# Optimization experiments

Measured on AMD Instinct MI355X. Metric: run time of the kernel, lower is better.

The kernel has to match this reference:

```python
import jax, jax.numpy as jnp
import numpy as np

Z1, COND, HID, NSTEP, B = 128, 12, 1024, 32, 4096


def setup_inputs() -> dict:
    key = jax.random.key(0)
    ks = jax.random.split(key, 10)
    s = 0.05  # init scale for learned params
    return {
        "z": jax.random.normal(ks[0], (B, Z1), jnp.float32),
        "condition": jax.random.uniform(ks[1], (B, NSTEP, COND), jnp.float32),
        "iteration": 1000,
        # nn.GRUCell params (gate order: r, z, n)
        "W_ih": jax.random.normal(ks[2], (3 * HID, Z1 + COND), jnp.float32) * s,
        "W_hh": jax.random.normal(ks[3], (3 * HID, HID), jnp.float32) * s,
        "b_ih": jax.random.normal(ks[4], (3 * HID,), jnp.float32) * s,
        "b_hh": jax.random.normal(ks[5], (3 * HID,), jnp.float32) * s,
        # linear_init_0
        "W_init": jax.random.normal(ks[6], (HID, Z1), jnp.float32) * s,
        "b_init": jax.random.normal(ks[7], (HID,), jnp.float32) * s,
        # linear_out_0
        "W_out": jax.random.normal(ks[8], (COND, HID), jnp.float32) * s,
        "b_out": jax.random.normal(ks[9], (COND,), jnp.float32) * s,
    }


def reference(z, condition, iteration, W_ih, W_hh, b_ih, b_hh, W_init, b_init, W_out, b_out):
    # Deterministic teacher-forcing path (training, eps=1): feedback at step i
    # is zeros for i=0, else condition[:, i-1, :]. iteration only affects the
    # stochastic eps schedule, which is dropped for determinism.
    del iteration
    b = z.shape[0]
    hx = jnp.tanh(z @ W_init.T + b_init)  # [B, H]
    feed = jnp.concatenate(
        [jnp.zeros((b, 1, COND), z.dtype), condition[:, :-1, :]], axis=1)  # [B, T, C]
    inputs = jnp.concatenate(
        [feed, jnp.broadcast_to(z[:, None, :], (b, NSTEP, z.shape[1]))], axis=-1)
    # precompute all input-to-hidden projections, time-major: [T, B, 3H]
    gi = jnp.einsum('bti,gi->tbg', inputs, W_ih) + b_ih

    def step(h, gi_t):
        gh = h @ W_hh.T + b_hh
        i_r, i_z, i_n = jnp.split(gi_t, 3, axis=-1)
        h_r, h_z, h_n = jnp.split(gh, 3, axis=-1)
        r = jax.nn.sigmoid(i_r + h_r)
        u = jax.nn.sigmoid(i_z + h_z)
        n = jnp.tanh(i_n + r * h_n)
        h_new = (1.0 - u) * n + u * h
        x = jax.nn.sigmoid(h_new @ W_out.T + b_out)  # [B, C]
        return h_new, x

    _, xs = jax.lax.scan(step, hx, gi)  # xs: [T, B, C]
    return jnp.transpose(xs, (1, 0, 2))  # [B, T, C]
```

## Files before the change

### kernel.cpp

```cpp
#include <hip/hip_runtime.h>
#include <stdint.h>

#define BB    4096
#define Z1D   128
#define CD    12
#define HD    1024
#define TT    32
#define N3H   3072
#define KAUG  1184
#define NGP   3168
#define NPH0B 1088

typedef __bf16 bf16;
typedef __bf16 bf16x2 __attribute__((ext_vector_type(2)));
typedef __bf16 bf16x8 __attribute__((ext_vector_type(8)));
typedef float  f32x4  __attribute__((ext_vector_type(4)));
typedef float  f4     __attribute__((ext_vector_type(4)));

typedef const __attribute__((address_space(1))) void* as1cv;
typedef __attribute__((address_space(3))) void* as3v;

__device__ __forceinline__ float sigm(float x){ return 1.0f/(1.0f+__expf(-x)); }
__device__ __forceinline__ float tanhfast(float x){ return 1.0f - 2.0f/(1.0f+__expf(2.0f*x)); }

__device__ __forceinline__ int rowOfN(int np, int& g){
  int jb = np/96; int r = np - jb*96; g = r>>5; int jl = r&31;
  return g*1024 + jb*32 + jl;
}

__global__ __launch_bounds__(256)
void prep_k(const float* __restrict__ z, const float* __restrict__ Wih,
            const float* __restrict__ Whh, const float* __restrict__ bih,
            const float* __restrict__ bhh, const float* __restrict__ Winit,
            const float* __restrict__ Wout,
            bf16* __restrict__ Wg, bf16* __restrict__ Wzn, bf16* __restrict__ Wi0,
            bf16* __restrict__ zbf, float* __restrict__ biasz,
            float* __restrict__ bhhn, float* __restrict__ bihn,
            bf16* __restrict__ A0, bf16* __restrict__ A1)
{
  const int N1 = NGP*KAUG;
  const int N2 = NPH0B*Z1D;
  const int N3 = NPH0B*Z1D;
  const int N4 = BB*Z1D;
  const int N5 = N3H;
  const int N6 = HD;
  const int N6b= HD;
  const int N7 = 2*BB*KAUG;
  int idx = blockIdx.x*256 + threadIdx.x;
  if (idx < N1){
    int np = idx/KAUG, k = idx - np*KAUG;
    float v = 0.0f;
    if (np < N3H){
      int g; int row = rowOfN(np, g);
      if (k < 1024) v = Whh[(size_t)row*HD + k];
      else if (g < 2){
        if (k < 1036)      v = Wih[(size_t)row*140 + (k-1024)];
        else if (k < 1164) v = Wih[(size_t)row*140 + 12 + (k-1036)];
      }
    } else {
      int c = np - N3H;
      if (c < CD && k < 1024) v = Wout[(size_t)c*HD + k];
    }
    Wg[idx] = (bf16)v;
    return;
  }
  idx -= N1;
  if (idx < N2){
    int jn = idx/Z1D, kk = idx - jn*Z1D;
    Wzn[idx] = (jn < HD) ? (bf16)Wih[(size_t)(2048+jn)*140 + 12 + kk] : (bf16)0.0f;
    return;
  }
  idx -= N2;
  if (idx < N3){
    int jn = idx/Z1D, kk = idx - jn*Z1D;
    Wi0[idx] = (jn < HD) ? (bf16)Winit[(size_t)jn*Z1D + kk] : (bf16)0.0f;
    return;
  }
  idx -= N3;
  if (idx < N4){ zbf[idx] = (bf16)z[idx]; return; }
  idx -= N4;
  if (idx < N5){
    int g; int row = rowOfN(idx, g);
    biasz[idx] = (g < 2) ? (bih[row] + bhh[row]) : 0.0f;
    return;
  }
  idx -= N5;
  if (idx < N6){ bhhn[idx] = bhh[2048 + idx]; return; }
  idx -= N6;
  if (idx < N6b){ bihn[idx] = bih[2048 + idx]; return; }
  idx -= N6b;
  if (idx < N7){
    int j = (idx < BB*KAUG) ? idx : idx - BB*KAUG;
    int b = j / KAUG, k = j - b*KAUG;
    bf16 v = (bf16)0.0f;
    if (k >= 1036 && k < 1164) v = (bf16)z[(size_t)b*Z1D + (k-1036)];
    if (idx < BB*KAUG) A0[j] = v; else A1[j] = v;
  }
}

template<int EP>
__global__ __launch_bounds__(256, 5)
void gemm_k(const bf16* __restrict__ A, int lda,
            const bf16* __restrict__ Bw, int ldb, int ksteps,
            const bf16* __restrict__ zpn, bf16* __restrict__ zpnw,
            const float* __restrict__ biasz, const float* __restrict__ bias1,
            const float* __restrict__ bhhn,
            const float* __restrict__ Wih, const float* __restrict__ cond,
            const bf16* __restrict__ Acur, bf16* __restrict__ Anext,
            const float* __restrict__ bout, float* __restrict__ outg, int t)
{
  __shared__ bf16 lA[2][128*32];
  __shared__ bf16 lB[2][96*32];
  const int tid = threadIdx.x, wid = tid>>6, lane = tid&63;
  const int l15 = lane&15, l4 = lane>>4;

  int bx, by;
  if constexpr (EP == 2){
    int bid = blockIdx.x;
    int x = bid & 7, k = bid >> 3;
    bx = k >> 2;
    by = x*4 + (k & 3);
  } else {
    bx = blockIdx.x; by = blockIdx.y;
  }
  const int n0 = bx*96, m0 = by*128;

  f32x4 acc[2][6];
  #pragma unroll
  for (int i=0;i<2;++i)
    #pragma unroll
    for (int j=0;j<6;++j) acc[i][j] = (f32x4){0.f,0.f,0.f,0.f};

  auto STAGE = [&](int buf, int ks){
    const int k0 = ks*32;
    const bf16* gA = A + (size_t)m0*lda + k0;
    #pragma unroll
    for (int r=0; r<2; ++r){
      int q = r*256 + tid;
      int row = q>>2, slot = q&3;
      int sg = slot ^ ((row>>1)&3);
      const bf16* gp = gA + (size_t)row*lda + sg*8;
      bf16* lp = &lA[buf][(size_t)(r*256 + wid*64)*8];
      __builtin_amdgcn_global_load_lds((as1cv)gp, (as3v)lp, 16, 0, 0);
    }
    const bf16* gB = Bw + (size_t)n0*ldb + k0;
    {
      int q = tid;
      int row = q>>2, slot = q&3;
      int sg = slot ^ ((row>>1)&3);
      const bf16* gp = gB + (size_t)row*ldb + sg*8;
      bf16* lp = &lB[buf][(size_t)(wid*64)*8];
      __builtin_amdgcn_global_load_lds((as1cv)gp, (as3v)lp, 16, 0, 0);
    }
    if (tid < 128){
      int q = 256 + tid;
      int row = q>>2, slot = q&3;
      int sg = slot ^ ((row>>1)&3);
      const bf16* gp = gB + (size_t)row*ldb + sg*8;
      bf16* lp = &lB[buf][(size_t)(256 + wid*64)*8];
      __builtin_amdgcn_global_load_lds((as1cv)gp, (as3v)lp, 16, 0, 0);
    }
  };

  const int sl = (l4 ^ ((l15>>1)&3))*8;

  int cur = 0;
  STAGE(0, 0);
  for (int ks=0; ks<ksteps; ++ks){
    __syncthreads();
    if (ks+1 < ksteps) STAGE(cur^1, ks+1);
    bf16x8 af0 = *(const bf16x8*)&lA[cur][(wid*32 +  0 + l15)*32 + sl];
    bf16x8 af1 = *(const bf16x8*)&lA[cur][(wid*32 + 16 + l15)*32 + sl];
    #pragma unroll
    for (int cf=0; cf<6; ++cf){
      bf16x8 bfr = *(const bf16x8*)&lB[cur][(cf*16 + l15)*32 + sl];
      acc[0][cf] = __builtin_amdgcn_mfma_f32_16x16x32_bf16(af0, bfr, acc[0][cf], 0,0,0);
      acc[1][cf] = __builtin_amdgcn_mfma_f32_16x16x32_bf16(af1, bfr, acc[1][cf], 0,0,0);
    }
    cur ^= 1;
  }

  const int rbase = m0 + wid*32 + l4*4;

  if constexpr (EP == 0){
    #pragma unroll
    for (int rf=0; rf<2; ++rf)
      #pragma unroll
      for (int cf=0; cf<6; ++cf){
        int jn = n0 + cf*16 + l15;
        if (jn < HD){
          float bi = bias1[jn];
          #pragma unroll
          for (int reg=0; reg<4; ++reg){
            int b = rbase + rf*16 + reg;
            zpnw[(size_t)b*HD + jn] = (bf16)(acc[rf][cf][reg] + bi);
          }
        }
      }
  }
  else if constexpr (EP == 1){
    #pragma unroll
    for (int rf=0; rf<2; ++rf)
      #pragma unroll
      for (int cf=0; cf<6; ++cf){
        int jn = n0 + cf*16 + l15;
        if (jn < HD){
          float bi = bias1[jn];
          #pragma unroll
          for (int reg=0; reg<4; ++reg){
            int b = rbase + rf*16 + reg;
            Anext[(size_t)b*KAUG + jn] = (bf16)tanhfast(acc[rf][cf][reg] + bi);
          }
        }
      }
  }
  else if (bx == 32){
    if (t > 0){
      int c = l15;
      if (c < CD){
        float bo = bout[c];
        #pragma unroll
        for (int rf=0; rf<2; ++rf){
          #pragma unroll
          for (int reg=0; reg<4; ++reg){
            int b = rbase + rf*16 + reg;
            outg[((size_t)b*TT + (t-1))*CD + c] = sigm(acc[rf][0][reg] + bo);
          }
        }
      }
    }
  }
  else {
    const int jblk = bx;
    float wfn[2][12];
    #pragma unroll
    for (int jf=0; jf<2; ++jf){
      int jn = jblk*32 + jf*16 + l15;
      const f4* wr = (const f4*)(Wih + (size_t)(2048 + jn)*140);
      f4 w0 = wr[0], w1 = wr[1], w2 = wr[2];
      #pragma unroll
      for (int c=0;c<4;++c){ wfn[jf][c]=w0[c]; wfn[jf][4+c]=w1[c]; wfn[jf][8+c]=w2[c]; }
    }
    #pragma unroll
    for (int rf=0; rf<2; ++rf){
      #pragma unroll
      for (int reg=0; reg<4; ++reg){
        int b = rbase + rf*16 + reg;
        const bf16* fr = Acur + (size_t)b*KAUG + 1024;
        bf16x8 f8 = *(const bf16x8*)fr;
        float fd[12];
        #pragma unroll
        for (int c=0;c<8;++c) fd[c] = (float)f8[c];
        #pragma unroll
        for (int c=8;c<12;++c) fd[c] = (float)fr[c];
        #pragma unroll
        for (int jf=0; jf<2; ++jf){
          int jn = jblk*32 + jf*16 + l15;
          int np = n0 + jf*16 + l15;
          float aR = acc[rf][jf  ][reg] + biasz[np];
          float aZ = acc[rf][2+jf][reg] + biasz[np+32];
          float hN = acc[rf][4+jf][reg] + bhhn[jn];
          float iN = (float)zpn[(size_t)b*HD + jn];
          float fdot = 0.0f;
          #pragma unroll
          for (int c=0;c<12;++c) fdot += fd[c]*wfn[jf][c];
          float r = sigm(aR);
          float u = sigm(aZ);
          float nn = tanhfast(iN + fdot + r*hN);
          float hp = (float)Acur[(size_t)b*KAUG + jn];
          float hv = (1.0f-u)*nn + u*hp;
          Anext[(size_t)b*KAUG + jn] = (bf16)hv;
        }
      }
    }
    if (jblk == 0){
      for (int i = tid; i < 128*CD; i += 256){
        int rr = i/CD, c = i - rr*CD;
        int b = m0 + rr;
        Anext[(size_t)b*KAUG + 1024 + c] = (bf16)cond[((size_t)b*TT + t)*CD + c];
      }
    }
  }
}

__global__ __launch_bounds__(256)
void out_k(const bf16* __restrict__ hstate, const float* __restrict__ Wout,
           const float* __restrict__ bout, float* __restrict__ out, int t)
{
  __shared__ float sw[CD*HD];
  __shared__ float sb[CD];
  const int tid = threadIdx.x;
  for (int i=tid; i<CD*HD; i+=256) sw[i] = Wout[i];
  if (tid < CD) sb[tid] = bout[tid];
  __syncthreads();
  const int wid = tid>>6, lane = tid&63;
  const int b0 = blockIdx.x*8 + wid*2;
  for (int rr=0; rr<2; ++rr){
    int b = b0 + rr;
    const bf16* hr = hstate + (size_t)b*KAUG;
    float p[CD];
    #pragma unroll
    for (int c=0;c<CD;++c) p[c] = 0.0f;
    #pragma unroll
    for (int j=0;j<8;++j){
      int idx = lane*2 + j*128;
      bf16x2 hv = *(const bf16x2*)&hr[idx];
      float h0 = (float)hv[0], h1 = (float)hv[1];
      #pragma unroll
      for (int c=0;c<CD;++c) p[c] += h0*sw[c*HD + idx] + h1*sw[c*HD + idx + 1];
    }
    #pragma unroll
    for (int c=0;c<CD;++c){
      float v = p[c];
      #pragma unroll
      for (int m=32;m>=1;m>>=1) v += __shfl_xor(v, m, 64);
      if (lane == 0) out[((size_t)b*TT + t)*CD + c] = sigm(v + sb[c]);
    }
  }
}

extern "C" void kernel_launch(void* const* d_in, const int* in_sizes, int n_in,
                              void* d_out, int out_size, void* d_ws, size_t ws_size,
                              hipStream_t stream) {
  const float* z     = (const float*)d_in[0];
  const float* cond  = (const float*)d_in[1];
  const float* Wih   = (const float*)d_in[3];
  const float* Whh   = (const float*)d_in[4];
  const float* bih   = (const float*)d_in[5];
  const float* bhh   = (const float*)d_in[6];
  const float* Winit = (const float*)d_in[7];
  const float* binit = (const float*)d_in[8];
  const float* Wout  = (const float*)d_in[9];
  const float* bout  = (const float*)d_in[10];
  float* out = (float*)d_out;

  char* ws = (char*)d_ws;
  size_t off = 0;
  auto carve = [&](size_t bytes)->char*{
    char* p = ws + off; off += (bytes + 255) & ~(size_t)255; return p;
  };
  bf16*  Wg    = (bf16*) carve((size_t)NGP*KAUG*2);
  bf16*  Wzn   = (bf16*) carve((size_t)NPH0B*Z1D*2);
  bf16*  Wi0   = (bf16*) carve((size_t)NPH0B*Z1D*2);
  bf16*  zbf   = (bf16*) carve((size_t)BB*Z1D*2);
  float* biasz = (float*)carve((size_t)N3H*4);
  float* bhhn  = (float*)carve((size_t)HD*4);
  float* bihn  = (float*)carve((size_t)HD*4);
  bf16*  zpn   = (bf16*) carve((size_t)BB*HD*2);
  bf16*  A0    = (bf16*) carve((size_t)BB*KAUG*2);
  bf16*  A1    = (bf16*) carve((size_t)BB*KAUG*2);

  {
    long total = (long)NGP*KAUG + 2L*NPH0B*Z1D + (long)BB*Z1D + N3H + 2*HD
               + 2L*BB*KAUG;
    int blocks = (int)((total + 255)/256);
    prep_k<<<blocks, 256, 0, stream>>>(z, Wih, Whh, bih, bhh, Winit, Wout,
                                       Wg, Wzn, Wi0, zbf, biasz, bhhn, bihn,
                                       A0, A1);
  }
  gemm_k<0><<<dim3(11,32), 256, 0, stream>>>(zbf, Z1D, Wzn, Z1D, 4,
      nullptr, zpn, nullptr, bihn, nullptr, nullptr, nullptr,
      nullptr, nullptr, nullptr, nullptr, 0);
  gemm_k<1><<<dim3(11,32), 256, 0, stream>>>(zbf, Z1D, Wi0, Z1D, 4,
      nullptr, nullptr, nullptr, binit, nullptr, nullptr, nullptr,
      nullptr, A0, nullptr, nullptr, 0);

  for (int t = 0; t < TT; ++t){
    const bf16* Ac = (t & 1) ? A1 : A0;
    bf16*       An = (t & 1) ? A0 : A1;
    gemm_k<2><<<1056, 256, 0, stream>>>(Ac, KAUG, Wg, KAUG, 37,
        zpn, nullptr, biasz, nullptr, bhhn, Wih, cond,
        Ac, An, bout, out, t);
  }
  out_k<<<512, 256, 0, stream>>>(A0, Wout, bout, out, 31);
}
```

Measured before the change: 1.926 ms.

## Stage GRU epilogue through LDS for vectorized bf16x8 loads and stores

The GRU gate epilogue now writes the MFMA accumulators into a shared-memory pool that reuses the GEMM staging buffers, then reads them back so each thread owns 8 contiguous hidden units of one batch row. zpn, h_prev and Anext are accessed as bf16x8 vectors, the biases as float4, and the n-gate feedback weights come from a new pre-transposed bf16 WfnT table instead of per-lane fp32 row gathers from Wih. This targets the scattered 2-byte global loads and stores in the epilogue, at the cost of extra barriers and an LDS round trip, and feedback weights are now rounded to bf16. NGP is padded to 3200, which enlarges the padded weight buffer.

```diff
diff --git a/kernel.cpp b/kernel.cpp
--- a/kernel.cpp
+++ b/kernel.cpp
@@ -8,7 +8,7 @@
 #define TT    32
 #define N3H   3072
 #define KAUG  1184
-#define NGP   3168
+#define NGP   3200
 #define NPH0B 1088
 
 typedef __bf16 bf16;
@@ -36,6 +36,7 @@
             bf16* __restrict__ Wg, bf16* __restrict__ Wzn, bf16* __restrict__ Wi0,
             bf16* __restrict__ zbf, float* __restrict__ biasz,
             float* __restrict__ bhhn, float* __restrict__ bihn,
+            bf16* __restrict__ WfnT,
             bf16* __restrict__ A0, bf16* __restrict__ A1)
 {
   const int N1 = NGP*KAUG;
@@ -45,6 +46,7 @@
   const int N5 = N3H;
   const int N6 = HD;
   const int N6b= HD;
+  const int N9 = CD*HD;
   const int N7 = 2*BB*KAUG;
   int idx = blockIdx.x*256 + threadIdx.x;
   if (idx < N1){
@@ -89,6 +91,12 @@
   idx -= N6;
   if (idx < N6b){ bihn[idx] = bih[2048 + idx]; return; }
   idx -= N6b;
+  if (idx < N9){
+    int c = idx/HD, j = idx - c*HD;
+    WfnT[idx] = (bf16)Wih[(size_t)(2048+j)*140 + c];
+    return;
+  }
+  idx -= N9;
   if (idx < N7){
     int j = (idx < BB*KAUG) ? idx : idx - BB*KAUG;
     int b = j / KAUG, k = j - b*KAUG;
@@ -105,12 +113,13 @@
             const bf16* __restrict__ zpn, bf16* __restrict__ zpnw,
             const float* __restrict__ biasz, const float* __restrict__ bias1,
             const float* __restrict__ bhhn,
-            const float* __restrict__ Wih, const float* __restrict__ cond,
+            const bf16* __restrict__ WfnT, const float* __restrict__ cond,
             const bf16* __restrict__ Acur, bf16* __restrict__ Anext,
             const float* __restrict__ bout, float* __restrict__ outg, int t)
 {
-  __shared__ bf16 lA[2][128*32];
-  __shared__ bf16 lB[2][96*32];
+  __shared__ __align__(16) char pool[28672];
+  bf16* lA = (bf16*)pool;
+  bf16* lB = (bf16*)(pool + 16384);
   const int tid = threadIdx.x, wid = tid>>6, lane = tid&63;
   const int l15 = lane&15, l4 = lane>>4;
 
@@ -134,22 +143,24 @@
   auto STAGE = [&](int buf, int ks){
     const int k0 = ks*32;
     const bf16* gA = A + (size_t)m0*lda + k0;
+    bf16* lAb = lA + buf*(128*32);
     #pragma unroll
     for (int r=0; r<2; ++r){
       int q = r*256 + tid;
       int row = q>>2, slot = q&3;
       int sg = slot ^ ((row>>1)&3);
       const bf16* gp = gA + (size_t)row*lda + sg*8;
-      bf16* lp = &lA[buf][(size_t)(r*256 + wid*64)*8];
+      bf16* lp = lAb + (size_t)(r*256 + wid*64)*8;
       __builtin_amdgcn_global_load_lds((as1cv)gp, (as3v)lp, 16, 0, 0);
     }
     const bf16* gB = Bw + (size_t)n0*ldb + k0;
+    bf16* lBb = lB + buf*(96*32);
     {
       int q = tid;
       int row = q>>2, slot = q&3;
       int sg = slot ^ ((row>>1)&3);
       const bf16* gp = gB + (size_t)row*ldb + sg*8;
-      bf16* lp = &lB[buf][(size_t)(wid*64)*8];
+      bf16* lp = lBb + (size_t)(wid*64)*8;
       __builtin_amdgcn_global_load_lds((as1cv)gp, (as3v)lp, 16, 0, 0);
     }
     if (tid < 128){
@@ -157,7 +168,7 @@
       int row = q>>2, slot = q&3;
       int sg = slot ^ ((row>>1)&3);
       const bf16* gp = gB + (size_t)row*ldb + sg*8;
-      bf16* lp = &lB[buf][(size_t)(256 + wid*64)*8];
+      bf16* lp = lBb + (size_t)(256 + wid*64)*8;
       __builtin_amdgcn_global_load_lds((as1cv)gp, (as3v)lp, 16, 0, 0);
     }
   };
@@ -169,11 +180,13 @@
   for (int ks=0; ks<ksteps; ++ks){
     __syncthreads();
     if (ks+1 < ksteps) STAGE(cur^1, ks+1);
-    bf16x8 af0 = *(const bf16x8*)&lA[cur][(wid*32 +  0 + l15)*32 + sl];
-    bf16x8 af1 = *(const bf16x8*)&lA[cur][(wid*32 + 16 + l15)*32 + sl];
+    const bf16* lAb = lA + cur*(128*32);
+    const bf16* lBb = lB + cur*(96*32);
+    bf16x8 af0 = *(const bf16x8*)&lAb[(wid*32 +  0 + l15)*32 + sl];
+    bf16x8 af1 = *(const bf16x8*)&lAb[(wid*32 + 16 + l15)*32 + sl];
     #pragma unroll
     for (int cf=0; cf<6; ++cf){
-      bf16x8 bfr = *(const bf16x8*)&lB[cur][(cf*16 + l15)*32 + sl];
+      bf16x8 bfr = *(const bf16x8*)&lBb[(cf*16 + l15)*32 + sl];
       acc[0][cf] = __builtin_amdgcn_mfma_f32_16x16x32_bf16(af0, bfr, acc[0][cf], 0,0,0);
       acc[1][cf] = __builtin_amdgcn_mfma_f32_16x16x32_bf16(af1, bfr, acc[1][cf], 0,0,0);
     }
@@ -232,46 +245,69 @@
   }
   else {
     const int jblk = bx;
-    float wfn[2][12];
-    #pragma unroll
-    for (int jf=0; jf<2; ++jf){
-      int jn = jblk*32 + jf*16 + l15;
-      const f4* wr = (const f4*)(Wih + (size_t)(2048 + jn)*140);
-      f4 w0 = wr[0], w1 = wr[1], w2 = wr[2];
-      #pragma unroll
-      for (int c=0;c<4;++c){ wfn[jf][c]=w0[c]; wfn[jf][4+c]=w1[c]; wfn[jf][8+c]=w2[c]; }
-    }
+    float* ep = (float*)pool;
     #pragma unroll
     for (int rf=0; rf<2; ++rf){
-      #pragma unroll
-      for (int reg=0; reg<4; ++reg){
-        int b = rbase + rf*16 + reg;
-        const bf16* fr = Acur + (size_t)b*KAUG + 1024;
-        bf16x8 f8 = *(const bf16x8*)fr;
-        float fd[12];
+      __syncthreads();
+      #pragma unroll
+      for (int cf=0; cf<6; ++cf){
+        int npl = cf*16 + l15;
         #pragma unroll
-        for (int c=0;c<8;++c) fd[c] = (float)f8[c];
+        for (int reg=0; reg<4; ++reg){
+          int lr = wid*16 + l4*4 + reg;
+          ep[lr*97 + npl] = acc[rf][cf][reg];
+        }
+      }
+      __syncthreads();
+      int lr = tid>>2;
+      int jo = (tid&3)*8;
+      int b  = m0 + (lr>>4)*32 + rf*16 + (lr&15);
+      int jn0 = jblk*32 + jo;
+      float rS[8], zS[8], nS[8];
+      #pragma unroll
+      for (int i=0;i<8;++i){
+        rS[i] = ep[lr*97 + jo + i];
+        zS[i] = ep[lr*97 + jo + 32 + i];
+        nS[i] = ep[lr*97 + jo + 64 + i];
+      }
+      bf16x8 zp8 = *(const bf16x8*)&zpn[(size_t)b*HD + jn0];
+      bf16x8 hp8 = *(const bf16x8*)&Acur[(size_t)b*KAUG + jn0];
+      const bf16* fr = Acur + (size_t)b*KAUG + 1024;
+      bf16x8 f8 = *(const bf16x8*)fr;
+      float fd[12];
+      #pragma unroll
+      for (int c=0;c<8;++c) fd[c] = (float)f8[c];
+      #pragma unroll
+      for (int c=8;c<12;++c) fd[c] = (float)fr[c];
+      float fdot[8];
+      #pragma unroll
+      for (int i=0;i<8;++i) fdot[i] = 0.0f;
+      #pragma unroll
+      for (int c=0;c<12;++c){
+        bf16x8 w8 = *(const bf16x8*)&WfnT[(size_t)c*HD + jn0];
         #pragma unroll
-        for (int c=8;c<12;++c) fd[c] = (float)fr[c];
-        #pragma unroll
-        for (int jf=0; jf<2; ++jf){
-          int jn = jblk*32 + jf*16 + l15;
-          int np = n0 + jf*16 + l15;
-          float aR = acc[rf][jf  ][reg] + biasz[np];
-          float aZ = acc[rf][2+jf][reg] + biasz[np+32];
-          float hN = acc[rf][4+jf][reg] + bhhn[jn];
-          float iN = (float)zpn[(size_t)b*HD + jn];
-          float fdot = 0.0f;
-          #pragma unroll
-          for (int c=0;c<12;++c) fdot += fd[c]*wfn[jf][c];
-          float r = sigm(aR);
-          float u = sigm(aZ);
-          float nn = tanhfast(iN + fdot + r*hN);
-          float hp = (float)Acur[(size_t)b*KAUG + jn];
-          float hv = (1.0f-u)*nn + u*hp;
-          Anext[(size_t)b*KAUG + jn] = (bf16)hv;
-        }
-      }
+        for (int i=0;i<8;++i) fdot[i] += fd[c]*(float)w8[i];
+      }
+      const f4* brp = (const f4*)&biasz[n0 + jo];
+      const f4* bzp = (const f4*)&biasz[n0 + 32 + jo];
+      const f4* bhp = (const f4*)&bhhn[jn0];
+      f4 br0 = brp[0], br1 = brp[1];
+      f4 bz0 = bzp[0], bz1 = bzp[1];
+      f4 bh0 = bhp[0], bh1 = bhp[1];
+      bf16 st[8];
+      #pragma unroll
+      for (int i=0;i<8;++i){
+        float brv = (i<4) ? br0[i] : br1[i-4];
+        float bzv = (i<4) ? bz0[i] : bz1[i-4];
+        float bhv = (i<4) ? bh0[i] : bh1[i-4];
+        float r = sigm(rS[i] + brv);
+        float u = sigm(zS[i] + bzv);
+        float iN = (float)zp8[i] + fdot[i];
+        float nn = tanhfast(iN + r*(nS[i] + bhv));
+        float hv = (1.0f-u)*nn + u*(float)hp8[i];
+        st[i] = (bf16)hv;
+      }
+      *(bf16x8*)&Anext[(size_t)b*KAUG + jn0] = *(bf16x8*)st;
     }
     if (jblk == 0){
       for (int i = tid; i < 128*CD; i += 256){
@@ -346,17 +382,18 @@
   float* biasz = (float*)carve((size_t)N3H*4);
   float* bhhn  = (float*)carve((size_t)HD*4);
   float* bihn  = (float*)carve((size_t)HD*4);
+  bf16*  WfnT  = (bf16*) carve((size_t)CD*HD*2);
   bf16*  zpn   = (bf16*) carve((size_t)BB*HD*2);
   bf16*  A0    = (bf16*) carve((size_t)BB*KAUG*2);
   bf16*  A1    = (bf16*) carve((size_t)BB*KAUG*2);
 
   {
     long total = (long)NGP*KAUG + 2L*NPH0B*Z1D + (long)BB*Z1D + N3H + 2*HD
-               + 2L*BB*KAUG;
+               + (long)CD*HD + 2L*BB*KAUG;
     int blocks = (int)((total + 255)/256);
     prep_k<<<blocks, 256, 0, stream>>>(z, Wih, Whh, bih, bhh, Winit, Wout,
                                        Wg, Wzn, Wi0, zbf, biasz, bhhn, bihn,
-                                       A0, A1);
+                                       WfnT, A0, A1);
   }
   gemm_k<0><<<dim3(11,32), 256, 0, stream>>>(zbf, Z1D, Wzn, Z1D, 4,
       nullptr, zpn, nullptr, bihn, nullptr, nullptr, nullptr,
@@ -369,7 +406,7 @@
     const bf16* Ac = (t & 1) ? A1 : A0;
     bf16*       An = (t & 1) ? A0 : A1;
     gemm_k<2><<<1056, 256, 0, stream>>>(Ac, KAUG, Wg, KAUG, 37,
-        zpn, nullptr, biasz, nullptr, bhhn, Wih, cond,
+        zpn, nullptr, biasz, nullptr, bhhn, WfnT, cond,
         Ac, An, bout, out, t);
   }
   out_k<<<512, 256, 0, stream>>>(A0, Wout, bout, out, 31);
```

Measured after the change: 2.115 ms. 9.8% more time.
